# Kernel optimization log

Measured on AMD Instinct MI355X. Metric: run time of the kernel, lower is better.

Reference implementation:

```python
import jax, jax.numpy as jnp
import numpy as np

B, T, D, H = 2, 2048, 1024, 16
Dh = D // H


def _rope(q, k):
    # q, k: (B, H, T, Dh), interleaved even/odd rotation
    t = q.shape[2]
    dh = q.shape[3]
    inv_freq = 1.0 / (10000.0 ** (jnp.arange(0, dh, 2, dtype=jnp.float32) / dh))
    pos = jnp.arange(t, dtype=jnp.float32)
    freqs = pos[:, None] * inv_freq[None, :]          # (T, Dh/2)
    sin = jnp.sin(freqs)[None, None]                  # (1,1,T,Dh/2)
    cos = jnp.cos(freqs)[None, None]

    def rot(x):
        xe, xo = x[..., ::2], x[..., 1::2]
        re = xe * cos - xo * sin
        ro = xe * sin + xo * cos
        return jnp.stack([re, ro], axis=-1).reshape(x.shape)

    return rot(q), rot(k)


def setup_inputs() -> dict:
    key = jax.random.key(0)
    k1, k2, k3 = jax.random.split(key, 3)
    s = 1.0 / np.sqrt(D)
    return {
        "x": jax.random.normal(k1, (B, T, D), dtype=jnp.float32),
        "w_qkv": jax.random.normal(k2, (3 * D, D), dtype=jnp.float32) * s,
        "b_qkv": jnp.zeros((3 * D,), dtype=jnp.float32),
        "w_out": jax.random.normal(k3, (D, D), dtype=jnp.float32) * s,
        "b_out": jnp.zeros((D,), dtype=jnp.float32),
    }


def reference(x, w_qkv, b_qkv, w_out, b_out):
    b, t, d = x.shape
    qkv = x @ w_qkv.T + b_qkv                         # (B,T,3D)
    q, k, v = jnp.split(qkv, 3, axis=-1)
    q = q.reshape(b, t, H, Dh).transpose(0, 2, 1, 3)  # (B,H,T,Dh)
    k = k.reshape(b, t, H, Dh).transpose(0, 2, 1, 3)
    v = v.reshape(b, t, H, Dh).transpose(0, 2, 1, 3)
    q, k = _rope(q, k)
    scores = jnp.einsum("bhtd,bhsd->bhts", q, k) / jnp.sqrt(jnp.float32(Dh))
    causal = jnp.tril(jnp.ones((t, t), dtype=bool))[None, None]
    scores = jnp.where(causal, scores, -jnp.inf)
    probs = jax.nn.softmax(scores, axis=-1)
    out = jnp.einsum("bhts,bhsd->bhtd", probs, v)     # (B,H,T,Dh)
    out = out.transpose(0, 2, 1, 3).reshape(b, t, d)
    return out @ w_out.T + b_out
```

## Files before the change

kernel.cpp:

```cpp
#include <hip/hip_runtime.h>
#include <hip/hip_bf16.h>
#include <math.h>
#include <type_traits>

#define B_ 2
#define T_ 2048
#define D_ 1024
#define H_ 16
#define DH_ 64

typedef __bf16 bf16_t;
typedef bf16_t bf16x8 __attribute__((ext_vector_type(8)));
typedef bf16_t bf16x4 __attribute__((ext_vector_type(4)));
typedef float f32x4 __attribute__((ext_vector_type(4)));

typedef __attribute__((address_space(1))) const void gas_void;
typedef __attribute__((address_space(3))) void las_void;

__device__ __forceinline__ void gld16(const void* g, void* l) {
    __builtin_amdgcn_global_load_lds((gas_void*)g, (las_void*)l, 16, 0, 0);
}

__global__ __launch_bounds__(256) void cvt3(const float* __restrict__ a,
                                            const float* __restrict__ b,
                                            const float* __restrict__ c,
                                            bf16_t* __restrict__ oa,
                                            bf16_t* __restrict__ ob,
                                            bf16_t* __restrict__ oc) {
    int i = blockIdx.x * 256 + threadIdx.x;
    const float* src; bf16_t* dst; int off;
    if (i < 1048576)      { src = a; dst = oa; off = i; }
    else if (i < 1835008) { src = b; dst = ob; off = i - 1048576; }
    else                  { src = c; dst = oc; off = i - 1835008; }
    float4 f = ((const float4*)src)[off];
    bf16x4 v = { (bf16_t)f.x, (bf16_t)f.y, (bf16_t)f.z, (bf16_t)f.w };
    ((bf16x4*)dst)[off] = v;
}

__global__ __launch_bounds__(256) void rope_tab_k(float2* __restrict__ tab) {
    int i = blockIdx.x * 256 + threadIdx.x;
    int t = i >> 5, d2 = i & 31;
    float invf = exp2f(-(float)d2 * 0.4152410118609203f);
    float ang = (float)t * invf;
    float sn, cs;
    sincosf(ang, &sn, &cs);
    tab[i] = make_float2(cs, sn);
}

template<int EPI>
__global__ __launch_bounds__(256) void gemm128(const bf16_t* __restrict__ A,
                                               const bf16_t* __restrict__ Bw,
                                               const float* __restrict__ bias,
                                               const float2* __restrict__ tab,
                                               bf16_t* __restrict__ q_out,
                                               bf16_t* __restrict__ k_out,
                                               bf16_t* __restrict__ vt_out,
                                               float* __restrict__ f_out,
                                               int K, int N) {
    __shared__ __align__(16) char smem[49152];
    char* b0 = smem;
    char* b1 = smem + 16384;
    char* b2 = smem + 32768;

    int tid = threadIdx.x;
    int lane = tid & 63, wid = tid >> 6;
    int wr = wid >> 1, wc = wid & 1;
    int lr = lane & 15, lk = lane >> 4;

    int l = blockIdx.y * gridDim.x + blockIdx.x;
    int chunk = (gridDim.x * gridDim.y) >> 3;
    int u = (l & 7) * chunk + (l >> 3);
    int bx = u % gridDim.x;
    int by = u / gridDim.x;

    f32x4 acc[4][4];
    f32x4 z = {0.f, 0.f, 0.f, 0.f};
#pragma unroll
    for (int i = 0; i < 4; i++)
#pragma unroll
        for (int j = 0; j < 4; j++) acc[i][j] = z;

    const char* Ab = (const char*)(A + (size_t)by * 128 * K);
    const char* Bb = (const char*)(Bw + (size_t)bx * 128 * K);
    const int rowstride = K * 2;

    int p0 = tid * 16;
    int p1 = 4096 + tid * 16;
    int r0 = p0 >> 6, r1 = p1 >> 6;
    int cb0 = (p0 & 63) ^ (((r0 >> 1) & 3) << 4);
    int cb1 = (p1 & 63) ^ (((r1 >> 1) & 3) << 4);
    size_t gA0 = (size_t)r0 * rowstride + cb0;
    size_t gA1 = (size_t)r1 * rowstride + cb1;

    int oa[4], ob[4];
#pragma unroll
    for (int m = 0; m < 4; m++) {
        int row = wr * 64 + m * 16 + lr;
        oa[m] = row * 64 + ((lk * 16) ^ (((row >> 1) & 3) << 4));
    }
#pragma unroll
    for (int n = 0; n < 4; n++) {
        int row = wc * 64 + n * 16 + lr;
        ob[n] = row * 64 + ((lk * 16) ^ (((row >> 1) & 3) << 4));
    }

    auto stg = [&](char* buf, int ks) __attribute__((always_inline)) {
        const char* Ag = Ab + (size_t)ks * 64;
        const char* Bg = Bb + (size_t)ks * 64;
        gld16(Ag + gA0, buf + p0);
        gld16(Ag + gA1, buf + p1);
        gld16(Bg + gA0, buf + 8192 + p0);
        gld16(Bg + gA1, buf + 8192 + p1);
    };

    auto iterf = [&](auto vmc, char* buf, int ks, bool dostage) __attribute__((always_inline)) {
        constexpr int VM = decltype(vmc)::value;
        if constexpr (VM == 8)      asm volatile("s_waitcnt vmcnt(8)" ::: "memory");
        else if constexpr (VM == 4) asm volatile("s_waitcnt vmcnt(4)" ::: "memory");
        else                        asm volatile("s_waitcnt vmcnt(0)" ::: "memory");
        __builtin_amdgcn_s_barrier();
        asm volatile("" ::: "memory");
        bf16x8 Af[4], Bf[4];
#pragma unroll
        for (int m = 0; m < 4; m++) Af[m] = *(const bf16x8*)(buf + oa[m]);
#pragma unroll
        for (int n = 0; n < 4; n++) Bf[n] = *(const bf16x8*)(buf + 8192 + ob[n]);
#pragma unroll
        for (int m = 0; m < 4; m++)
#pragma unroll
            for (int n = 0; n < 4; n++)
                acc[m][n] = __builtin_amdgcn_mfma_f32_16x16x32_bf16(Af[m], Bf[n], acc[m][n], 0, 0, 0);
        asm volatile("" ::: "memory");
        __builtin_amdgcn_s_barrier();
        asm volatile("" ::: "memory");
        if (dostage) stg(buf, ks);
    };

    std::integral_constant<int, 8> c8;
    std::integral_constant<int, 4> c4;
    std::integral_constant<int, 0> c0;

    stg(b0, 0);
    stg(b1, 1);
    stg(b2, 2);
    for (int s = 0; s < 30; s += 3) {
        iterf(c8, b0, s + 3, s + 3 < 32);
        iterf(c8, b1, s + 4, s + 4 < 32);
        iterf(c8, b2, s + 5, s + 5 < 32);
    }
    iterf(c4, b0, 0, false);
    iterf(c0, b1, 0, false);

    int m_base = by * 128 + wr * 64;
    int n_base = bx * 128 + wc * 64;
    if (EPI == 1) {
#pragma unroll
        for (int m = 0; m < 4; m++) {
            int gm0 = m_base + m * 16 + lk * 4;
#pragma unroll
            for (int n = 0; n < 4; n++) {
                int nc = n_base + n * 16 + lr;
                float bv = bias[nc];
#pragma unroll
                for (int j = 0; j < 4; j++)
                    f_out[(size_t)(gm0 + j) * N + nc] = acc[m][n][j] + bv;
            }
        }
    } else {
        char* myL = smem + wid * 8192;
        int which = n_base >> 10;
        int h = (n_base & 1023) >> 6;
        int b = m_base >> 11, t0 = m_base & 2047;
        int bh = b * H_ + h;
        if (which == 2) {
#pragma unroll
            for (int m = 0; m < 4; m++)
#pragma unroll
                for (int n = 0; n < 4; n++) {
                    int rd = n * 16 + lr;
                    float bv = bias[n_base + rd];
#pragma unroll
                    for (int j = 0; j < 4; j++) {
                        int ct = m * 16 + lk * 4 + j;
                        int ct2 = (ct & 32) | (((ct >> 2) & 3) << 3) | (((ct >> 4) & 1) << 2) | (ct & 3);
                        int addr = (rd * 128 + ct2 * 2) ^ ((rd & 7) << 4);
                        *(bf16_t*)(myL + addr) = (bf16_t)(acc[m][n][j] + bv);
                    }
                }
#pragma unroll
            for (int it = 0; it < 8; it++) {
                int row = it * 8 + (lane >> 3);
                int byte = (lane & 7) * 16;
                bf16x8 val = *(const bf16x8*)(myL + ((row * 128 + byte) ^ ((row & 7) << 4)));
                *(bf16x8*)(vt_out + ((size_t)bh * DH_ + row) * T_ + t0 + (lane & 7) * 8) = val;
            }
        } else {
            bf16_t* dst = which ? k_out : q_out;
#pragma unroll
            for (int m = 0; m < 4; m++)
#pragma unroll
                for (int n = 0; n < 4; n++) {
                    int dh = n * 16 + lr;
                    float bv = bias[n_base + dh];
                    int dh2 = dh >> 1;
                    bool even = (dh & 1) == 0;
#pragma unroll
                    for (int j = 0; j < 4; j++) {
                        int rt = m * 16 + lk * 4 + j;
                        float v = acc[m][n][j] + bv;
                        float p = __shfl_xor(v, 1);
                        float2 cs = tab[(t0 + rt) * 32 + dh2];
                        float r = even ? v * cs.x - p * cs.y : v * cs.x + p * cs.y;
                        int addr = (rt * 128 + dh * 2) ^ ((rt & 7) << 4);
                        *(bf16_t*)(myL + addr) = (bf16_t)r;
                    }
                }
#pragma unroll
            for (int it = 0; it < 8; it++) {
                int row = it * 8 + (lane >> 3);
                int byte = (lane & 7) * 16;
                bf16x8 val = *(const bf16x8*)(myL + ((row * 128 + byte) ^ ((row & 7) << 4)));
                *(bf16x8*)(dst + ((size_t)bh * T_ + t0 + row) * DH_ + (lane & 7) * 8) = val;
            }
        }
    }
}

__global__ __launch_bounds__(256) void attn64(const bf16_t* __restrict__ Q,
                                              const bf16_t* __restrict__ K,
                                              const bf16_t* __restrict__ Vt,
                                              bf16_t* __restrict__ Ao) {
    __shared__ char smem[32768];

    int tid = threadIdx.x;
    int lane = tid & 63, wid = tid >> 6;
    int lr = lane & 15, lk = lane >> 4;
    int xcd = blockIdx.x & 7, idx = blockIdx.x >> 3;
    int bh = xcd * 4 + (idx & 3);
    int qt = idx >> 2;
    int q0 = qt * 64;
    int qrel = wid * 16 + lr;

    const bf16_t* Qp = Q + ((size_t)bh * T_ + q0 + qrel) * DH_;
    bf16x8 qf0 = *(const bf16x8*)(Qp + lk * 8);
    bf16x8 qf1 = *(const bf16x8*)(Qp + 32 + lk * 8);

    f32x4 zz = {0.f, 0.f, 0.f, 0.f};
    f32x4 oacc[4];
#pragma unroll
    for (int dt = 0; dt < 4; dt++) oacc[dt] = zz;
    float mrun = -__builtin_inff(), lsum = 0.f;

    const char* Kbase = (const char*)(K + (size_t)bh * T_ * DH_);
    const char* Vbase = (const char*)(Vt + (size_t)bh * DH_ * T_);

    auto stage = [&](int s, char* Kd, char* Vd) {
        int kv0 = s * 64;
        const char* Kg = Kbase + (size_t)kv0 * 128;
#pragma unroll
        for (int c = 0; c < 2; c++) {
            int o = c * 4096 + tid * 16;
            int r = o >> 7;
            int g = o ^ ((r & 7) << 4);
            gld16(Kg + g, Kd + o);
            gld16(Vbase + (size_t)r * (T_ * 2) + kv0 * 2 + (g & 127), Vd + o);
        }
    };

    const float SCL2 = 0.18033688011112042f;

    auto compute = [&](const char* Kc, const char* Vc, bool dmask) __attribute__((always_inline)) {
        float p[4][4];
#pragma unroll
        for (int kt = 0; kt < 4; kt++) {
            int row = kt * 16 + lr;
            int key = (row & 7) << 4;
            bf16x8 kf0 = *(const bf16x8*)(Kc + ((row * 128 + lk * 16) ^ key));
            bf16x8 kf1 = *(const bf16x8*)(Kc + ((row * 128 + 64 + lk * 16) ^ key));
            f32x4 sacc = zz;
            sacc = __builtin_amdgcn_mfma_f32_16x16x32_bf16(kf0, qf0, sacc, 0, 0, 0);
            sacc = __builtin_amdgcn_mfma_f32_16x16x32_bf16(kf1, qf1, sacc, 0, 0, 0);
#pragma unroll
            for (int j = 0; j < 4; j++) {
                float sv = sacc[j] * SCL2;
                if (dmask) {
                    int kvrel = kt * 16 + lk * 4 + j;
                    sv = (kvrel <= qrel) ? sv : -__builtin_inff();
                }
                p[kt][j] = sv;
            }
        }
        float mx = p[0][0];
#pragma unroll
        for (int kt = 0; kt < 4; kt++)
#pragma unroll
            for (int j = 0; j < 4; j++) mx = fmaxf(mx, p[kt][j]);
        mx = fmaxf(mx, __shfl_xor(mx, 16));
        mx = fmaxf(mx, __shfl_xor(mx, 32));
        float mnew = fmaxf(mrun, mx);
        float fac = exp2f(mrun - mnew);
        mrun = mnew;
        float rs = 0.f;
#pragma unroll
        for (int kt = 0; kt < 4; kt++)
#pragma unroll
            for (int j = 0; j < 4; j++) {
                float e = exp2f(p[kt][j] - mnew);
                p[kt][j] = e;
                rs += e;
            }
        rs += __shfl_xor(rs, 16);
        rs += __shfl_xor(rs, 32);
        lsum = lsum * fac + rs;
        bf16x8 pb0 = { (bf16_t)p[0][0], (bf16_t)p[0][1], (bf16_t)p[0][2], (bf16_t)p[0][3],
                       (bf16_t)p[1][0], (bf16_t)p[1][1], (bf16_t)p[1][2], (bf16_t)p[1][3] };
        bf16x8 pb1 = { (bf16_t)p[2][0], (bf16_t)p[2][1], (bf16_t)p[2][2], (bf16_t)p[2][3],
                       (bf16_t)p[3][0], (bf16_t)p[3][1], (bf16_t)p[3][2], (bf16_t)p[3][3] };
#pragma unroll
        for (int dt = 0; dt < 4; dt++) {
            f32x4 o = oacc[dt];
            o[0] *= fac; o[1] *= fac; o[2] *= fac; o[3] *= fac;
            int row = dt * 16 + lr;
            int key = (row & 7) << 4;
            bf16x8 vf0 = *(const bf16x8*)(Vc + ((row * 128 + lk * 16) ^ key));
            bf16x8 vf1 = *(const bf16x8*)(Vc + ((row * 128 + 64 + lk * 16) ^ key));
            o = __builtin_amdgcn_mfma_f32_16x16x32_bf16(vf0, pb0, o, 0, 0, 0);
            o = __builtin_amdgcn_mfma_f32_16x16x32_bf16(vf1, pb1, o, 0, 0, 0);
            oacc[dt] = o;
        }
    };

    stage(0, smem, smem + 16384);
    __syncthreads();
    for (int s = 0; s < qt; ++s) {
        char* Kc = smem + ((s & 1) ? 8192 : 0);
        char* Vc = smem + 16384 + ((s & 1) ? 8192 : 0);
        char* Kn = smem + ((s & 1) ? 0 : 8192);
        char* Vn = smem + 16384 + ((s & 1) ? 0 : 8192);
        stage(s + 1, Kn, Vn);
        compute(Kc, Vc, false);
        __syncthreads();
    }
    {
        char* Kc = smem + ((qt & 1) ? 8192 : 0);
        char* Vc = smem + 16384 + ((qt & 1) ? 8192 : 0);
        compute(Kc, Vc, true);
    }
    __syncthreads();

    char* myL = smem + wid * 2048;
    float rinv = __builtin_amdgcn_rcpf(lsum);
#pragma unroll
    for (int dt = 0; dt < 4; dt++)
#pragma unroll
        for (int j = 0; j < 4; j++) {
            int dh = dt * 16 + lk * 4 + j;
            int addr = (lr * 128 + dh * 2) ^ ((lr & 7) << 4);
            *(bf16_t*)(myL + addr) = (bf16_t)(oacc[dt][j] * rinv);
        }
    int b = bh >> 4, h = bh & 15;
#pragma unroll
    for (int it = 0; it < 2; it++) {
        int row = it * 8 + (lane >> 3);
        int byte = (lane & 7) * 16;
        bf16x8 val = *(const bf16x8*)(myL + ((row * 128 + byte) ^ ((row & 7) << 4)));
        int t = q0 + wid * 16 + row;
        *(bf16x8*)(Ao + ((size_t)b * T_ + t) * D_ + h * DH_ + (lane & 7) * 8) = val;
    }
}

extern "C" void kernel_launch(void* const* d_in, const int* in_sizes, int n_in,
                              void* d_out, int out_size, void* d_ws, size_t ws_size,
                              hipStream_t stream) {
    const float* x     = (const float*)d_in[0];
    const float* w_qkv = (const float*)d_in[1];
    const float* b_qkv = (const float*)d_in[2];
    const float* w_out = (const float*)d_in[3];
    const float* b_out = (const float*)d_in[4];
    float* out = (float*)d_out;

    char* ws = (char*)d_ws;
    bf16_t* xb    = (bf16_t*)(ws);
    bf16_t* wqkvb = (bf16_t*)(ws + 8388608);
    bf16_t* wob   = (bf16_t*)(ws + 14680064);
    bf16_t* qb    = (bf16_t*)(ws + 16777216);
    bf16_t* kb    = (bf16_t*)(ws + 25165824);
    bf16_t* vtb   = (bf16_t*)(ws + 33554432);
    bf16_t* ab    = (bf16_t*)(ws + 41943040);
    float2* tab   = (float2*)(ws + 41943040);

    rope_tab_k<<<256, 256, 0, stream>>>(tab);
    cvt3<<<8192, 256, 0, stream>>>(x, w_qkv, w_out, xb, wqkvb, wob);

    gemm128<0><<<dim3(24, 32), 256, 0, stream>>>(xb, wqkvb, b_qkv, tab, qb, kb, vtb, nullptr, 1024, 3072);
    attn64<<<1024, 256, 0, stream>>>(qb, kb, vtb, ab);
    gemm128<1><<<dim3(8, 32), 256, 0, stream>>>(ab, wob, b_out, nullptr, nullptr, nullptr, nullptr, out, 1024, 1024);
}
```

Before: 126.0 us.

## Software-pipeline QK/PV in attention with lazy rescale and balanced causal tile order

Restructures the attention loop so the QK product for the next KV tile is issued alongside the PV product for the previous tile, using a triple-buffered V and double-buffered K shared-memory layout and waitcnt-based barriers. The softmax scale is folded into Q inside the projection epilogue, which removes a per-score multiply. Online-softmax rescaling is skipped unless the running max grows by more than a threshold. Query tiles are also remapped in a zig-zag order to balance causal work across blocks, and occupancy is hinted with launch bounds. Together these raise LDS use and code complexity, and the lazy rescale relies on exp2 headroom staying within fp32 range.

New measurement: 115.9 us. 1.09x faster.

```diff
diff --git a/kernel.cpp b/kernel.cpp
--- a/kernel.cpp
+++ b/kernel.cpp
@@ -196,6 +196,7 @@
             }
         } else {
             bf16_t* dst = which ? k_out : q_out;
+            float qscl = which ? 1.0f : 0.18033688011112042f;
 #pragma unroll
             for (int m = 0; m < 4; m++)
 #pragma unroll
@@ -211,6 +212,7 @@
                         float p = __shfl_xor(v, 1);
                         float2 cs = tab[(t0 + rt) * 32 + dh2];
                         float r = even ? v * cs.x - p * cs.y : v * cs.x + p * cs.y;
+                        r *= qscl;
                         int addr = (rt * 128 + dh * 2) ^ ((rt & 7) << 4);
                         *(bf16_t*)(myL + addr) = (bf16_t)r;
                     }
@@ -226,18 +228,20 @@
     }
 }
 
-__global__ __launch_bounds__(256) void attn64(const bf16_t* __restrict__ Q,
-                                              const bf16_t* __restrict__ K,
-                                              const bf16_t* __restrict__ Vt,
-                                              bf16_t* __restrict__ Ao) {
-    __shared__ char smem[32768];
+__global__ __launch_bounds__(256, 4) void attn64(const bf16_t* __restrict__ Q,
+                                                 const bf16_t* __restrict__ K,
+                                                 const bf16_t* __restrict__ Vt,
+                                                 bf16_t* __restrict__ Ao) {
+    __shared__ __align__(16) char smem[40960];
 
     int tid = threadIdx.x;
     int lane = tid & 63, wid = tid >> 6;
     int lr = lane & 15, lk = lane >> 4;
     int xcd = blockIdx.x & 7, idx = blockIdx.x >> 3;
     int bh = xcd * 4 + (idx & 3);
-    int qt = idx >> 2;
+    int i5 = idx >> 2;
+    int qq = i5 & 7, rr = i5 >> 3;
+    int qt = (rr == 0) ? qq : (rr == 1) ? 15 - qq : (rr == 2) ? 16 + qq : 31 - qq;
     int q0 = qt * 64;
     int qrel = wid * 16 + lr;
 
@@ -254,7 +258,7 @@
     const char* Kbase = (const char*)(K + (size_t)bh * T_ * DH_);
     const char* Vbase = (const char*)(Vt + (size_t)bh * DH_ * T_);
 
-    auto stage = [&](int s, char* Kd, char* Vd) {
+    auto stage = [&](int s, char* Kd, char* Vd) __attribute__((always_inline)) {
         int kv0 = s * 64;
         const char* Kg = Kbase + (size_t)kv0 * 128;
 #pragma unroll
@@ -267,10 +271,11 @@
         }
     };
 
-    const float SCL2 = 0.18033688011112042f;
-
-    auto compute = [&](const char* Kc, const char* Vc, bool dmask) __attribute__((always_inline)) {
-        float p[4][4];
+    float p[4][4];
+    bf16x8 pb0, pb1;
+
+    auto do_qk = [&](const char* Kc, auto dmc) __attribute__((always_inline)) {
+        constexpr bool DM = decltype(dmc)::value;
 #pragma unroll
         for (int kt = 0; kt < 4; kt++) {
             int row = kt * 16 + lr;
@@ -282,70 +287,97 @@
             sacc = __builtin_amdgcn_mfma_f32_16x16x32_bf16(kf1, qf1, sacc, 0, 0, 0);
 #pragma unroll
             for (int j = 0; j < 4; j++) {
-                float sv = sacc[j] * SCL2;
-                if (dmask) {
+                if (DM) {
                     int kvrel = kt * 16 + lk * 4 + j;
-                    sv = (kvrel <= qrel) ? sv : -__builtin_inff();
+                    p[kt][j] = (kvrel <= qrel) ? sacc[j] : -__builtin_inff();
+                } else {
+                    p[kt][j] = sacc[j];
                 }
-                p[kt][j] = sv;
             }
         }
-        float mx = p[0][0];
+    };
+
+    auto do_pv = [&](const char* Vc) __attribute__((always_inline)) {
+#pragma unroll
+        for (int dt = 0; dt < 4; dt++) {
+            int row = dt * 16 + lr;
+            int key = (row & 7) << 4;
+            bf16x8 vf0 = *(const bf16x8*)(Vc + ((row * 128 + lk * 16) ^ key));
+            bf16x8 vf1 = *(const bf16x8*)(Vc + ((row * 128 + 64 + lk * 16) ^ key));
+            f32x4 o = oacc[dt];
+            o = __builtin_amdgcn_mfma_f32_16x16x32_bf16(vf0, pb0, o, 0, 0, 0);
+            o = __builtin_amdgcn_mfma_f32_16x16x32_bf16(vf1, pb1, o, 0, 0, 0);
+            oacc[dt] = o;
+        }
+    };
+
+    auto do_softmax = [&]() __attribute__((always_inline)) {
+        float mk[4];
 #pragma unroll
         for (int kt = 0; kt < 4; kt++)
-#pragma unroll
-            for (int j = 0; j < 4; j++) mx = fmaxf(mx, p[kt][j]);
+            mk[kt] = fmaxf(fmaxf(p[kt][0], p[kt][1]), fmaxf(p[kt][2], p[kt][3]));
+        float mx = fmaxf(fmaxf(mk[0], mk[1]), fmaxf(mk[2], mk[3]));
         mx = fmaxf(mx, __shfl_xor(mx, 16));
         mx = fmaxf(mx, __shfl_xor(mx, 32));
-        float mnew = fmaxf(mrun, mx);
-        float fac = exp2f(mrun - mnew);
-        mrun = mnew;
+        if (!__all(mx <= mrun + 8.f)) {
+            float mnew = fmaxf(mrun, mx);
+            float fac = exp2f(mrun - mnew);
+            mrun = mnew;
+            lsum *= fac;
+#pragma unroll
+            for (int dt = 0; dt < 4; dt++) oacc[dt] = oacc[dt] * fac;
+        }
         float rs = 0.f;
 #pragma unroll
         for (int kt = 0; kt < 4; kt++)
 #pragma unroll
             for (int j = 0; j < 4; j++) {
-                float e = exp2f(p[kt][j] - mnew);
+                float e = exp2f(p[kt][j] - mrun);
                 p[kt][j] = e;
                 rs += e;
             }
         rs += __shfl_xor(rs, 16);
         rs += __shfl_xor(rs, 32);
-        lsum = lsum * fac + rs;
-        bf16x8 pb0 = { (bf16_t)p[0][0], (bf16_t)p[0][1], (bf16_t)p[0][2], (bf16_t)p[0][3],
-                       (bf16_t)p[1][0], (bf16_t)p[1][1], (bf16_t)p[1][2], (bf16_t)p[1][3] };
-        bf16x8 pb1 = { (bf16_t)p[2][0], (bf16_t)p[2][1], (bf16_t)p[2][2], (bf16_t)p[2][3],
-                       (bf16_t)p[3][0], (bf16_t)p[3][1], (bf16_t)p[3][2], (bf16_t)p[3][3] };
-#pragma unroll
-        for (int dt = 0; dt < 4; dt++) {
-            f32x4 o = oacc[dt];
-            o[0] *= fac; o[1] *= fac; o[2] *= fac; o[3] *= fac;
-            int row = dt * 16 + lr;
-            int key = (row & 7) << 4;
-            bf16x8 vf0 = *(const bf16x8*)(Vc + ((row * 128 + lk * 16) ^ key));
-            bf16x8 vf1 = *(const bf16x8*)(Vc + ((row * 128 + 64 + lk * 16) ^ key));
-            o = __builtin_amdgcn_mfma_f32_16x16x32_bf16(vf0, pb0, o, 0, 0, 0);
-            o = __builtin_amdgcn_mfma_f32_16x16x32_bf16(vf1, pb1, o, 0, 0, 0);
-            oacc[dt] = o;
-        }
-    };
+        lsum += rs;
+        pb0 = bf16x8{ (bf16_t)p[0][0], (bf16_t)p[0][1], (bf16_t)p[0][2], (bf16_t)p[0][3],
+                      (bf16_t)p[1][0], (bf16_t)p[1][1], (bf16_t)p[1][2], (bf16_t)p[1][3] };
+        pb1 = bf16x8{ (bf16_t)p[2][0], (bf16_t)p[2][1], (bf16_t)p[2][2], (bf16_t)p[2][3],
+                      (bf16_t)p[3][0], (bf16_t)p[3][1], (bf16_t)p[3][2], (bf16_t)p[3][3] };
+    };
+
+    std::integral_constant<bool, true>  mask_y;
+    std::integral_constant<bool, false> mask_n;
 
     stage(0, smem, smem + 16384);
-    __syncthreads();
-    for (int s = 0; s < qt; ++s) {
-        char* Kc = smem + ((s & 1) ? 8192 : 0);
-        char* Vc = smem + 16384 + ((s & 1) ? 8192 : 0);
-        char* Kn = smem + ((s & 1) ? 0 : 8192);
-        char* Vn = smem + 16384 + ((s & 1) ? 0 : 8192);
-        stage(s + 1, Kn, Vn);
-        compute(Kc, Vc, false);
-        __syncthreads();
-    }
-    {
-        char* Kc = smem + ((qt & 1) ? 8192 : 0);
-        char* Vc = smem + 16384 + ((qt & 1) ? 8192 : 0);
-        compute(Kc, Vc, true);
-    }
+    stage(1, smem + 8192, smem + 24576);
+    asm volatile("s_waitcnt vmcnt(4)" ::: "memory");
+    __builtin_amdgcn_s_barrier();
+    asm volatile("" ::: "memory");
+    if (qt == 0) do_qk(smem, mask_y); else do_qk(smem, mask_n);
+    do_softmax();
+
+    char* Kr = smem + 8192;
+    char* Kw = smem;
+    char* Vr = smem + 16384;
+    char* Vn = smem + 24576;
+    char* Vw = smem + 32768;
+
+    auto iter = [&](int s, auto dmc) __attribute__((always_inline)) {
+        asm volatile("s_waitcnt vmcnt(0)" ::: "memory");
+        __builtin_amdgcn_s_barrier();
+        asm volatile("" ::: "memory");
+        if (s + 2 <= qt) stage(s + 2, Kw, Vw);
+        do_qk(Kr, dmc);
+        do_pv(Vr);
+        do_softmax();
+        char* t;
+        t = Kr; Kr = Kw; Kw = t;
+        t = Vr; Vr = Vn; Vn = Vw; Vw = t;
+    };
+
+    for (int s = 0; s + 1 < qt; ++s) iter(s, mask_n);
+    if (qt > 0) iter(qt - 1, mask_y);
+    do_pv(Vr);
     __syncthreads();
 
     char* myL = smem + wid * 2048;
```
